# Optimization experiments

Measured on AMD Instinct MI355X. Metric: run time of the kernel, lower is better.

The kernel has to match this reference:

```python
import jax, jax.numpy as jnp
import numpy as np

N_SRC0, N_DST0 = 100000, 20000   # block0: 100k src -> 20k dst
N_DST1 = 4096                    # block1: 20k src -> 4096 dst (seed nodes)


def setup_inputs() -> dict:
    key = jax.random.key(0)
    ks = jax.random.split(key, 8)
    E0, E1 = 640000, 131072
    return {
        "features": jax.random.normal(ks[0], (N_SRC0, 256), jnp.float32),
        "W1": jax.random.normal(ks[1], (256, 256), jnp.float32) * (1.0 / np.sqrt(256)),
        "b1": jnp.zeros((256,), jnp.float32),
        "W2": jax.random.normal(ks[2], (256, 128), jnp.float32) * (1.0 / np.sqrt(256)),
        "b2": jnp.zeros((128,), jnp.float32),
        "src0": jax.random.randint(ks[3], (E0,), 0, N_SRC0, jnp.int32),
        "dst0": jax.random.randint(ks[4], (E0,), 0, N_DST0, jnp.int32),
        "src1": jax.random.randint(ks[5], (E1,), 0, N_DST0, jnp.int32),
        "dst1": jax.random.randint(ks[6], (E1,), 0, N_DST1, jnp.int32),
    }


def _graph_conv(src, dst, n_dst, feat, W, b):
    # DGL GraphConv, norm='both': D_out^{-1/2} gather-sum D_in^{-1/2}, then WX+b.
    n_src = feat.shape[0]
    ones = jnp.ones(src.shape[0], feat.dtype)
    out_deg = jax.ops.segment_sum(ones, src, num_segments=n_src)
    norm_src = jnp.clip(out_deg, 1.0, None) ** -0.5          # [n_src]
    h = feat * norm_src[:, None]
    agg = jax.ops.segment_sum(h[src], dst, num_segments=n_dst)  # sparse SpMM
    in_deg = jax.ops.segment_sum(ones, dst, num_segments=n_dst)
    norm_dst = jnp.clip(in_deg, 1.0, None) ** -0.5           # [n_dst]
    return (agg * norm_dst[:, None]) @ W + b


def reference(features, W1, b1, W2, b2, src0, dst0, src1, dst1):
    x = jax.nn.relu(_graph_conv(src0, dst0, N_DST0, features, W1, b1))
    x = _graph_conv(src1, dst1, N_DST1, x, W2, b2)
    return x
```

## Files before the change

kernel.cpp:

```cpp
#include <hip/hip_runtime.h>
#include <hip/hip_bf16.h>

#define K_DIM 256
#define RSTRIDE 128

typedef short bf16x8 __attribute__((ext_vector_type(8)));
typedef float f32x4 __attribute__((ext_vector_type(4)));

static __device__ __forceinline__ unsigned short f2bf(float x) {
    __hip_bfloat16 b = __float2bfloat16(x);
    return *reinterpret_cast<unsigned short*>(&b);
}
static __device__ __forceinline__ float bflo(unsigned int p) {
    return __uint_as_float(p << 16);
}
static __device__ __forceinline__ float bfhi(unsigned int p) {
    return __uint_as_float(p & 0xffff0000u);
}

__global__ void mega_kernel(
        const int* __restrict__ src0, const int* __restrict__ dst0,
        int* __restrict__ od0, int* __restrict__ cnt0, int* __restrict__ esrc0, int E0,
        const int* __restrict__ src1, const int* __restrict__ dst1,
        int* __restrict__ od1, int* __restrict__ cnt1, int* __restrict__ esrc1, int E1,
        int edgeBlocks,
        const float* __restrict__ feat, unsigned short* __restrict__ h, int total_f,
        int castBlocks,
        const float* __restrict__ W1, uint4* __restrict__ pw1,
        const float* __restrict__ W2, uint4* __restrict__ pw2) {
    const int b = blockIdx.x;
    if (b < edgeBlocks) {
        int i = b * blockDim.x + threadIdx.x;
        if (i < E0) {
            int s = src0[i];
            int d = dst0[i];
            atomicAdd(&od0[s], 1);
            int slot = atomicAdd(&cnt0[d], 1);
            if (slot < RSTRIDE) esrc0[(d << 7) + slot] = s;
        } else if (i < E0 + E1) {
            int e = i - E0;
            int s = src1[e];
            int d = dst1[e];
            atomicAdd(&od1[s], 1);
            int slot = atomicAdd(&cnt1[d], 1);
            if (slot < RSTRIDE) esrc1[(d << 7) + slot] = s;
        }
    } else if (b < edgeBlocks + castBlocks) {
        int idx = ((b - edgeBlocks) * blockDim.x + threadIdx.x) * 8;
        if (idx >= total_f) return;
        const float4 v0 = *reinterpret_cast<const float4*>(feat + idx);
        const float4 v1 = *reinterpret_cast<const float4*>(feat + idx + 4);
        union { ushort4 u4[2]; uint4 u; } o;
        o.u4[0].x = f2bf(v0.x); o.u4[0].y = f2bf(v0.y);
        o.u4[0].z = f2bf(v0.z); o.u4[0].w = f2bf(v0.w);
        o.u4[1].x = f2bf(v1.x); o.u4[1].y = f2bf(v1.y);
        o.u4[1].z = f2bf(v1.z); o.u4[1].w = f2bf(v1.w);
        *reinterpret_cast<uint4*>(h + idx) = o.u;
    } else if (b < edgeBlocks + castBlocks + 32) {
        int idx = (b - edgeBlocks - castBlocks) * blockDim.x + threadIdx.x;
        int lane = idx & 63;
        int kt = (idx >> 6) & 7;
        int nt = idx >> 9;
        int n = nt * 16 + (lane & 15);
        int k = kt * 32 + (lane >> 4) * 8;
        union { unsigned short us[8]; uint4 u; } o;
#pragma unroll
        for (int j = 0; j < 8; ++j) o.us[j] = f2bf(W1[(size_t)(k + j) * 256 + n]);
        pw1[idx] = o.u;
    } else {
        int idx = (b - edgeBlocks - castBlocks - 32) * blockDim.x + threadIdx.x;
        int lane = idx & 63;
        int kt = (idx >> 6) & 7;
        int nt = idx >> 9;
        int n = nt * 16 + (lane & 15);
        int k = kt * 32 + (lane >> 4) * 8;
        union { unsigned short us[8]; uint4 u; } o;
#pragma unroll
        for (int j = 0; j < 8; ++j) o.us[j] = f2bf(W2[(size_t)(k + j) * 128 + n]);
        pw2[idx] = o.u;
    }
}

template <bool NORM>
__global__ __launch_bounds__(256) void gather_bf16_kernel(
        const unsigned short* __restrict__ hfeat, const int* __restrict__ esrc,
        const int* __restrict__ cnt, const int* __restrict__ od,
        unsigned short* __restrict__ aggb, int n_dst) {
    int row = blockIdx.x * (blockDim.x >> 6) + (threadIdx.x >> 6);
    int lane = threadIdx.x & 63;
    if (row >= n_dst) return;
    const int c = cnt[row];
    const int cend = min(c, RSTRIDE);
    const int* __restrict__ ep = esrc + ((size_t)row << 7);
    float a0 = 0.f, a1 = 0.f, a2 = 0.f, a3 = 0.f;
    int i = 0;
    for (; i + 3 < cend; i += 4) {
        int s0 = ep[i];
        int s1 = ep[i + 1];
        int s2 = ep[i + 2];
        int s3 = ep[i + 3];
        float n0 = NORM ? rsqrtf((float)max(od[s0], 1)) : 1.0f;
        float n1 = NORM ? rsqrtf((float)max(od[s1], 1)) : 1.0f;
        float n2 = NORM ? rsqrtf((float)max(od[s2], 1)) : 1.0f;
        float n3 = NORM ? rsqrtf((float)max(od[s3], 1)) : 1.0f;
        const uint2 p0 = *reinterpret_cast<const uint2*>(hfeat + (((size_t)s0) << 8) + lane * 4);
        const uint2 p1 = *reinterpret_cast<const uint2*>(hfeat + (((size_t)s1) << 8) + lane * 4);
        const uint2 p2 = *reinterpret_cast<const uint2*>(hfeat + (((size_t)s2) << 8) + lane * 4);
        const uint2 p3 = *reinterpret_cast<const uint2*>(hfeat + (((size_t)s3) << 8) + lane * 4);
        if (NORM) {
            a0 = fmaf(bflo(p0.x), n0, a0); a1 = fmaf(bfhi(p0.x), n0, a1);
            a2 = fmaf(bflo(p0.y), n0, a2); a3 = fmaf(bfhi(p0.y), n0, a3);
            a0 = fmaf(bflo(p1.x), n1, a0); a1 = fmaf(bfhi(p1.x), n1, a1);
            a2 = fmaf(bflo(p1.y), n1, a2); a3 = fmaf(bfhi(p1.y), n1, a3);
            a0 = fmaf(bflo(p2.x), n2, a0); a1 = fmaf(bfhi(p2.x), n2, a1);
            a2 = fmaf(bflo(p2.y), n2, a2); a3 = fmaf(bfhi(p2.y), n2, a3);
            a0 = fmaf(bflo(p3.x), n3, a0); a1 = fmaf(bfhi(p3.x), n3, a1);
            a2 = fmaf(bflo(p3.y), n3, a2); a3 = fmaf(bfhi(p3.y), n3, a3);
        } else {
            a0 += (bflo(p0.x) + bflo(p1.x)) + (bflo(p2.x) + bflo(p3.x));
            a1 += (bfhi(p0.x) + bfhi(p1.x)) + (bfhi(p2.x) + bfhi(p3.x));
            a2 += (bflo(p0.y) + bflo(p1.y)) + (bflo(p2.y) + bflo(p3.y));
            a3 += (bfhi(p0.y) + bfhi(p1.y)) + (bfhi(p2.y) + bfhi(p3.y));
        }
    }
    for (; i < cend; ++i) {
        int s0 = ep[i];
        float n0 = NORM ? rsqrtf((float)max(od[s0], 1)) : 1.0f;
        const uint2 p0 = *reinterpret_cast<const uint2*>(hfeat + (((size_t)s0) << 8) + lane * 4);
        if (NORM) {
            a0 = fmaf(bflo(p0.x), n0, a0); a1 = fmaf(bfhi(p0.x), n0, a1);
            a2 = fmaf(bflo(p0.y), n0, a2); a3 = fmaf(bfhi(p0.y), n0, a3);
        } else {
            a0 += bflo(p0.x);
            a1 += bfhi(p0.x);
            a2 += bflo(p0.y);
            a3 += bfhi(p0.y);
        }
    }
    float nd = rsqrtf((float)max(c, 1));
    ushort4 o;
    o.x = f2bf(a0 * nd);
    o.y = f2bf(a1 * nd);
    o.z = f2bf(a2 * nd);
    o.w = f2bf(a3 * nd);
    *reinterpret_cast<ushort4*>(aggb + (((size_t)row) << 8) + lane * 4) = o;
}

__global__ __launch_bounds__(256) void gemm0_mfma_kernel(
        const unsigned short* __restrict__ hA, const uint4* __restrict__ pW,
        const float* __restrict__ bias, const int* __restrict__ od1,
        unsigned short* __restrict__ out, int M) {
    const int m0 = blockIdx.x * 16;
    const int w = threadIdx.x >> 6;
    const int lane = threadIdx.x & 63;

    bf16x8 a[8];
    const unsigned short* ap = hA + (size_t)(m0 + (lane & 15)) * K_DIM + (lane >> 4) * 8;
#pragma unroll
    for (int kt = 0; kt < 8; ++kt)
        a[kt] = *reinterpret_cast<const bf16x8*>(ap + kt * 32);

    const int rbase = m0 + (lane >> 4) * 4;
    float nsv[4];
#pragma unroll
    for (int r = 0; r < 4; ++r) nsv[r] = rsqrtf((float)max(od1[rbase + r], 1));

#pragma unroll
    for (int nt = 0; nt < 4; ++nt) {
        const int n0 = w * 64 + nt * 16;
        f32x4 acc = {0.f, 0.f, 0.f, 0.f};
#pragma unroll
        for (int kt = 0; kt < 8; ++kt) {
            bf16x8 b = *reinterpret_cast<const bf16x8*>(&pW[((size_t)(n0 >> 4) * 8 + kt) * 64 + lane]);
            acc = __builtin_amdgcn_mfma_f32_16x16x32_bf16(a[kt], b, acc, 0, 0, 0);
        }
        const int col = n0 + (lane & 15);
        const float bv = bias[col];
#pragma unroll
        for (int r = 0; r < 4; ++r) {
            float v = fmaxf(acc[r] + bv, 0.0f) * nsv[r];
            out[(size_t)(rbase + r) * K_DIM + col] = f2bf(v);
        }
    }
}

__global__ __launch_bounds__(256) void gemm1_mfma_kernel(
        const unsigned short* __restrict__ hA, const uint4* __restrict__ pW,
        const float* __restrict__ bias, float* __restrict__ out, int M) {
    const int m0 = blockIdx.x * 16;
    const int w = threadIdx.x >> 6;
    const int lane = threadIdx.x & 63;

    bf16x8 a[8];
    const unsigned short* ap = hA + (size_t)(m0 + (lane & 15)) * K_DIM + (lane >> 4) * 8;
#pragma unroll
    for (int kt = 0; kt < 8; ++kt)
        a[kt] = *reinterpret_cast<const bf16x8*>(ap + kt * 32);

    const int rbase = m0 + (lane >> 4) * 4;
#pragma unroll
    for (int nt = 0; nt < 2; ++nt) {
        const int n0 = w * 32 + nt * 16;
        f32x4 acc = {0.f, 0.f, 0.f, 0.f};
#pragma unroll
        for (int kt = 0; kt < 8; ++kt) {
            bf16x8 b = *reinterpret_cast<const bf16x8*>(&pW[((size_t)(n0 >> 4) * 8 + kt) * 64 + lane]);
            acc = __builtin_amdgcn_mfma_f32_16x16x32_bf16(a[kt], b, acc, 0, 0, 0);
        }
        const int col = n0 + (lane & 15);
        const float bv = bias[col];
#pragma unroll
        for (int r = 0; r < 4; ++r)
            out[(size_t)(rbase + r) * 128 + col] = acc[r] + bv;
    }
}

__global__ __launch_bounds__(256) void gatherf_kernel(
        const float* __restrict__ feat, const int* __restrict__ esrc,
        const int* __restrict__ cnt, const int* __restrict__ od,
        float* __restrict__ outbuf, int n_dst) {
    int row = blockIdx.x * (blockDim.x >> 6) + (threadIdx.x >> 6);
    int lane = threadIdx.x & 63;
    if (row >= n_dst) return;
    const int c = cnt[row];
    const int cend = min(c, RSTRIDE);
    const int* __restrict__ ep = esrc + ((size_t)row << 7);
    float4 acc = {0.f, 0.f, 0.f, 0.f};
    for (int i = 0; i < cend; ++i) {
        int s0 = ep[i];
        float n0 = rsqrtf((float)max(od[s0], 1));
        const float4 v0 = *reinterpret_cast<const float4*>(feat + (((size_t)s0) << 8) + lane * 4);
        acc.x = fmaf(v0.x, n0, acc.x); acc.y = fmaf(v0.y, n0, acc.y);
        acc.z = fmaf(v0.z, n0, acc.z); acc.w = fmaf(v0.w, n0, acc.w);
    }
    float nd = rsqrtf((float)max(c, 1));
    float4 o = {acc.x * nd, acc.y * nd, acc.z * nd, acc.w * nd};
    *reinterpret_cast<float4*>(outbuf + (((size_t)row) << 8) + lane * 4) = o;
}

__global__ void edges_kernel(const int* __restrict__ src0, const int* __restrict__ dst0,
                             int* __restrict__ od0, int* __restrict__ cnt0,
                             int* __restrict__ esrc0, int E0,
                             const int* __restrict__ src1, const int* __restrict__ dst1,
                             int* __restrict__ od1, int* __restrict__ cnt1,
                             int* __restrict__ esrc1, int E1) {
    int i = blockIdx.x * blockDim.x + threadIdx.x;
    if (i < E0) {
        int s = src0[i];
        int d = dst0[i];
        atomicAdd(&od0[s], 1);
        int slot = atomicAdd(&cnt0[d], 1);
        if (slot < RSTRIDE) esrc0[(d << 7) + slot] = s;
    } else if (i < E0 + E1) {
        int e = i - E0;
        int s = src1[e];
        int d = dst1[e];
        atomicAdd(&od1[s], 1);
        int slot = atomicAdd(&cnt1[d], 1);
        if (slot < RSTRIDE) esrc1[(d << 7) + slot] = s;
    }
}

template <int ROWS, int NCOLS, bool RELU>
__global__ __launch_bounds__(NCOLS) void gemm_kernel(
        const float* __restrict__ A, const float* __restrict__ W,
        const float* __restrict__ bias, float* __restrict__ out, int M) {
    const int row0 = blockIdx.x * ROWS;
    const int c = threadIdx.x;
    const float* __restrict__ Ablk = A + (size_t)row0 * K_DIM;
    const float* __restrict__ Wc = W + c;

    float acc[ROWS];
#pragma unroll
    for (int r = 0; r < ROWS; ++r) acc[r] = 0.0f;

    float w0 = Wc[0];
    float w1 = Wc[NCOLS];
    float w2 = Wc[2 * NCOLS];
    float w3 = Wc[3 * NCOLS];

#pragma unroll 2
    for (int k = 0; k < K_DIM - 4; k += 4) {
        const float* p = Wc + (size_t)(k + 4) * NCOLS;
        float n0 = p[0];
        float n1 = p[NCOLS];
        float n2 = p[2 * NCOLS];
        float n3 = p[3 * NCOLS];
#pragma unroll
        for (int r = 0; r < ROWS; ++r) {
            const float4 a = *reinterpret_cast<const float4*>(Ablk + r * K_DIM + k);
            acc[r] = fmaf(a.x, w0, acc[r]);
            acc[r] = fmaf(a.y, w1, acc[r]);
            acc[r] = fmaf(a.z, w2, acc[r]);
            acc[r] = fmaf(a.w, w3, acc[r]);
        }
        w0 = n0; w1 = n1; w2 = n2; w3 = n3;
    }
    {
        const int k = K_DIM - 4;
#pragma unroll
        for (int r = 0; r < ROWS; ++r) {
            const float4 a = *reinterpret_cast<const float4*>(Ablk + r * K_DIM + k);
            acc[r] = fmaf(a.x, w0, acc[r]);
            acc[r] = fmaf(a.y, w1, acc[r]);
            acc[r] = fmaf(a.z, w2, acc[r]);
            acc[r] = fmaf(a.w, w3, acc[r]);
        }
    }

    const float b = bias[c];
#pragma unroll
    for (int r = 0; r < ROWS; ++r) {
        float v = acc[r] + b;
        if (RELU) v = fmaxf(v, 0.0f);
        out[(size_t)(row0 + r) * NCOLS + c] = v;
    }
}

extern "C" void kernel_launch(void* const* d_in, const int* in_sizes, int n_in,
                              void* d_out, int out_size, void* d_ws, size_t ws_size,
                              hipStream_t stream) {
    const float* features = (const float*)d_in[0];
    const float* W1 = (const float*)d_in[1];
    const float* b1 = (const float*)d_in[2];
    const float* W2 = (const float*)d_in[3];
    const float* b2 = (const float*)d_in[4];
    const int* src0 = (const int*)d_in[5];
    const int* dst0 = (const int*)d_in[6];
    const int* src1 = (const int*)d_in[7];
    const int* dst1 = (const int*)d_in[8];
    const int E0 = in_sizes[5];
    const int E1 = in_sizes[7];
    const int NSRC0 = 100000, NDST0 = 20000, NDST1 = 4096;

    char* ws = (char*)d_ws;
    size_t off = 0;
    auto carve = [&](size_t bytes) -> void* {
        void* p = ws + off;
        off = (off + bytes + 255) & ~(size_t)255;
        return p;
    };
    int* od0  = (int*)carve((size_t)NSRC0 * 4);
    int* od1  = (int*)carve((size_t)NDST0 * 4);
    int* cnt0 = (int*)carve((size_t)NDST0 * 4);
    int* cnt1 = (int*)carve((size_t)NDST1 * 4);
    const size_t zero_span = off;
    uint4* pW1  = (uint4*)carve((size_t)8192 * 16);
    uint4* pW2  = (uint4*)carve((size_t)4096 * 16);
    int* esrc0p = (int*)carve((size_t)NDST0 * RSTRIDE * 4);
    int* esrc1p = (int*)carve((size_t)NDST1 * RSTRIDE * 4);
    unsigned short* aggb = (unsigned short*)carve((size_t)NDST0 * K_DIM * 2);
    const size_t hfeat_bytes = (size_t)NSRC0 * K_DIM * 2;
    const size_t xbufb_bytes = (size_t)NDST0 * K_DIM * 2;
    const size_t agg1b_bytes = (size_t)NDST1 * K_DIM * 2;
    const size_t need_bf16 = off + (hfeat_bytes > xbufb_bytes + agg1b_bytes
                                        ? hfeat_bytes : xbufb_bytes + agg1b_bytes);
    (void)n_in; (void)out_size;

    hipMemsetAsync(ws, 0, zero_span, stream);

    if (ws_size >= need_bf16) {
        unsigned short* hfeat = (unsigned short*)(ws + off);
        unsigned short* xbufb = (unsigned short*)(ws + off);
        unsigned short* agg1b = (unsigned short*)(ws + off + xbufb_bytes);

        const int total_f = NSRC0 * K_DIM;
        const int edgeBlocks = (E0 + E1 + 255) / 256;
        const int castBlocks = (total_f / 8 + 255) / 256;
        mega_kernel<<<edgeBlocks + castBlocks + 48, 256, 0, stream>>>(
            src0, dst0, od0, cnt0, esrc0p, E0,
            src1, dst1, od1, cnt1, esrc1p, E1, edgeBlocks,
            features, hfeat, total_f, castBlocks,
            W1, pW1, W2, pW2);
        gather_bf16_kernel<true><<<(NDST0 + 3) / 4, 256, 0, stream>>>(
            hfeat, esrc0p, cnt0, od0, aggb, NDST0);
        gemm0_mfma_kernel<<<NDST0 / 16, 256, 0, stream>>>(aggb, pW1, b1, od1, xbufb, NDST0);
        gather_bf16_kernel<false><<<(NDST1 + 3) / 4, 256, 0, stream>>>(
            xbufb, esrc1p, cnt1, nullptr, agg1b, NDST1);
        gemm1_mfma_kernel<<<NDST1 / 16, 256, 0, stream>>>(agg1b, pW2, b2,
                                                          (float*)d_out, NDST1);
    } else {
        float* agg0 = (float*)carve((size_t)NDST0 * K_DIM * 4);
        float* xbuf = (float*)carve((size_t)NDST0 * K_DIM * 4);
        float* agg1 = (float*)carve((size_t)NDST1 * K_DIM * 4);
        edges_kernel<<<(E0 + E1 + 255) / 256, 256, 0, stream>>>(
            src0, dst0, od0, cnt0, esrc0p, E0,
            src1, dst1, od1, cnt1, esrc1p, E1);
        gatherf_kernel<<<(NDST0 + 3) / 4, 256, 0, stream>>>(features, esrc0p, cnt0, od0,
                                                            agg0, NDST0);
        gemm_kernel<16, 256, true><<<NDST0 / 16, 256, 0, stream>>>(agg0, W1, b1, xbuf, NDST0);
        gatherf_kernel<<<(NDST1 + 3) / 4, 256, 0, stream>>>(xbuf, esrc1p, cnt1, od1,
                                                            agg1, NDST1);
        gemm_kernel<4, 128, false><<<NDST1 / 4, 128, 0, stream>>>(agg1, W2, b2,
                                                                  (float*)d_out, NDST1);
    }
}
```

Measured before the change: 314.8 us.

## Privatize degree counters and edge lists per XCD with workgroup-scope atomics

```diff
diff --git a/kernel.cpp b/kernel.cpp
--- a/kernel.cpp
+++ b/kernel.cpp
@@ -2,6 +2,8 @@
 #include <hip/hip_bf16.h>
 
 #define K_DIM 256
+#define XCDS 8
+#define PSTRIDE 32
 #define RSTRIDE 128
 
 typedef short bf16x8 __attribute__((ext_vector_type(8)));
@@ -17,33 +19,43 @@
 static __device__ __forceinline__ float bfhi(unsigned int p) {
     return __uint_as_float(p & 0xffff0000u);
 }
+static __device__ __forceinline__ unsigned xcc_id() {
+    unsigned x;
+    asm volatile("s_getreg_b32 %0, hwreg(HW_REG_XCC_ID)" : "=s"(x));
+    return x & 7;
+}
+static __device__ __forceinline__ int l2_atomic_add(int* p) {
+    return __hip_atomic_fetch_add(p, 1, __ATOMIC_RELAXED, __HIP_MEMORY_SCOPE_WORKGROUP);
+}
 
 __global__ void mega_kernel(
         const int* __restrict__ src0, const int* __restrict__ dst0,
-        int* __restrict__ od0, int* __restrict__ cnt0, int* __restrict__ esrc0, int E0,
+        int* __restrict__ od0x, int* __restrict__ cnt0x, int* __restrict__ esrc0, int E0,
         const int* __restrict__ src1, const int* __restrict__ dst1,
-        int* __restrict__ od1, int* __restrict__ cnt1, int* __restrict__ esrc1, int E1,
+        int* __restrict__ od1x, int* __restrict__ cnt1x, int* __restrict__ esrc1, int E1,
         int edgeBlocks,
         const float* __restrict__ feat, unsigned short* __restrict__ h, int total_f,
         int castBlocks,
         const float* __restrict__ W1, uint4* __restrict__ pw1,
         const float* __restrict__ W2, uint4* __restrict__ pw2) {
     const int b = blockIdx.x;
+    const int NSRC0 = 100000, NDST0 = 20000, NDST1 = 4096;
     if (b < edgeBlocks) {
+        const unsigned x = xcc_id();
         int i = b * blockDim.x + threadIdx.x;
         if (i < E0) {
             int s = src0[i];
             int d = dst0[i];
-            atomicAdd(&od0[s], 1);
-            int slot = atomicAdd(&cnt0[d], 1);
-            if (slot < RSTRIDE) esrc0[(d << 7) + slot] = s;
+            l2_atomic_add(&od0x[x * NSRC0 + s]);
+            int slot = l2_atomic_add(&cnt0x[x * NDST0 + d]);
+            if (slot < PSTRIDE) esrc0[(((size_t)(x * NDST0 + d)) << 5) + slot] = s;
         } else if (i < E0 + E1) {
             int e = i - E0;
             int s = src1[e];
             int d = dst1[e];
-            atomicAdd(&od1[s], 1);
-            int slot = atomicAdd(&cnt1[d], 1);
-            if (slot < RSTRIDE) esrc1[(d << 7) + slot] = s;
+            l2_atomic_add(&od1x[x * NDST0 + s]);
+            int slot = l2_atomic_add(&cnt1x[x * NDST1 + d]);
+            if (slot < PSTRIDE) esrc1[(((size_t)(x * NDST1 + d)) << 5) + slot] = s;
         }
     } else if (b < edgeBlocks + castBlocks) {
         int idx = ((b - edgeBlocks) * blockDim.x + threadIdx.x) * 8;
@@ -81,6 +93,23 @@
     }
 }
 
+__global__ void reduce8_kernel(const int* __restrict__ od0x, int* __restrict__ od0s, int n0,
+                               const int* __restrict__ od1x, int* __restrict__ od1s, int n1) {
+    int i = blockIdx.x * blockDim.x + threadIdx.x;
+    if (i < n0) {
+        int s = 0;
+#pragma unroll
+        for (int x = 0; x < XCDS; ++x) s += od0x[x * n0 + i];
+        od0s[i] = s;
+    } else if (i < n0 + n1) {
+        int j = i - n0;
+        int s = 0;
+#pragma unroll
+        for (int x = 0; x < XCDS; ++x) s += od1x[x * n1 + j];
+        od1s[j] = s;
+    }
+}
+
 template <bool NORM>
 __global__ __launch_bounds__(256) void gather_bf16_kernel(
         const unsigned short* __restrict__ hfeat, const int* __restrict__ esrc,
@@ -89,55 +118,59 @@
     int row = blockIdx.x * (blockDim.x >> 6) + (threadIdx.x >> 6);
     int lane = threadIdx.x & 63;
     if (row >= n_dst) return;
-    const int c = cnt[row];
-    const int cend = min(c, RSTRIDE);
-    const int* __restrict__ ep = esrc + ((size_t)row << 7);
     float a0 = 0.f, a1 = 0.f, a2 = 0.f, a3 = 0.f;
-    int i = 0;
-    for (; i + 3 < cend; i += 4) {
-        int s0 = ep[i];
-        int s1 = ep[i + 1];
-        int s2 = ep[i + 2];
-        int s3 = ep[i + 3];
-        float n0 = NORM ? rsqrtf((float)max(od[s0], 1)) : 1.0f;
-        float n1 = NORM ? rsqrtf((float)max(od[s1], 1)) : 1.0f;
-        float n2 = NORM ? rsqrtf((float)max(od[s2], 1)) : 1.0f;
-        float n3 = NORM ? rsqrtf((float)max(od[s3], 1)) : 1.0f;
-        const uint2 p0 = *reinterpret_cast<const uint2*>(hfeat + (((size_t)s0) << 8) + lane * 4);
-        const uint2 p1 = *reinterpret_cast<const uint2*>(hfeat + (((size_t)s1) << 8) + lane * 4);
-        const uint2 p2 = *reinterpret_cast<const uint2*>(hfeat + (((size_t)s2) << 8) + lane * 4);
-        const uint2 p3 = *reinterpret_cast<const uint2*>(hfeat + (((size_t)s3) << 8) + lane * 4);
-        if (NORM) {
-            a0 = fmaf(bflo(p0.x), n0, a0); a1 = fmaf(bfhi(p0.x), n0, a1);
-            a2 = fmaf(bflo(p0.y), n0, a2); a3 = fmaf(bfhi(p0.y), n0, a3);
-            a0 = fmaf(bflo(p1.x), n1, a0); a1 = fmaf(bfhi(p1.x), n1, a1);
-            a2 = fmaf(bflo(p1.y), n1, a2); a3 = fmaf(bfhi(p1.y), n1, a3);
-            a0 = fmaf(bflo(p2.x), n2, a0); a1 = fmaf(bfhi(p2.x), n2, a1);
-            a2 = fmaf(bflo(p2.y), n2, a2); a3 = fmaf(bfhi(p2.y), n2, a3);
-            a0 = fmaf(bflo(p3.x), n3, a0); a1 = fmaf(bfhi(p3.x), n3, a1);
-            a2 = fmaf(bflo(p3.y), n3, a2); a3 = fmaf(bfhi(p3.y), n3, a3);
-        } else {
-            a0 += (bflo(p0.x) + bflo(p1.x)) + (bflo(p2.x) + bflo(p3.x));
-            a1 += (bfhi(p0.x) + bfhi(p1.x)) + (bfhi(p2.x) + bfhi(p3.x));
-            a2 += (bflo(p0.y) + bflo(p1.y)) + (bflo(p2.y) + bflo(p3.y));
-            a3 += (bfhi(p0.y) + bfhi(p1.y)) + (bfhi(p2.y) + bfhi(p3.y));
-        }
-    }
-    for (; i < cend; ++i) {
-        int s0 = ep[i];
-        float n0 = NORM ? rsqrtf((float)max(od[s0], 1)) : 1.0f;
-        const uint2 p0 = *reinterpret_cast<const uint2*>(hfeat + (((size_t)s0) << 8) + lane * 4);
-        if (NORM) {
-            a0 = fmaf(bflo(p0.x), n0, a0); a1 = fmaf(bfhi(p0.x), n0, a1);
-            a2 = fmaf(bflo(p0.y), n0, a2); a3 = fmaf(bfhi(p0.y), n0, a3);
-        } else {
-            a0 += bflo(p0.x);
-            a1 += bfhi(p0.x);
-            a2 += bflo(p0.y);
-            a3 += bfhi(p0.y);
-        }
-    }
-    float nd = rsqrtf((float)max(c, 1));
+    int ctot = 0;
+#pragma unroll
+    for (int x = 0; x < XCDS; ++x) {
+        const int cx = min(cnt[x * n_dst + row], PSTRIDE);
+        ctot += cx;
+        const int* __restrict__ ep = esrc + (((size_t)(x * n_dst + row)) << 5);
+        int i = 0;
+        for (; i + 3 < cx; i += 4) {
+            int s0 = ep[i];
+            int s1 = ep[i + 1];
+            int s2 = ep[i + 2];
+            int s3 = ep[i + 3];
+            float n0 = NORM ? rsqrtf((float)max(od[s0], 1)) : 1.0f;
+            float n1 = NORM ? rsqrtf((float)max(od[s1], 1)) : 1.0f;
+            float n2 = NORM ? rsqrtf((float)max(od[s2], 1)) : 1.0f;
+            float n3 = NORM ? rsqrtf((float)max(od[s3], 1)) : 1.0f;
+            const uint2 p0 = *reinterpret_cast<const uint2*>(hfeat + (((size_t)s0) << 8) + lane * 4);
+            const uint2 p1 = *reinterpret_cast<const uint2*>(hfeat + (((size_t)s1) << 8) + lane * 4);
+            const uint2 p2 = *reinterpret_cast<const uint2*>(hfeat + (((size_t)s2) << 8) + lane * 4);
+            const uint2 p3 = *reinterpret_cast<const uint2*>(hfeat + (((size_t)s3) << 8) + lane * 4);
+            if (NORM) {
+                a0 = fmaf(bflo(p0.x), n0, a0); a1 = fmaf(bfhi(p0.x), n0, a1);
+                a2 = fmaf(bflo(p0.y), n0, a2); a3 = fmaf(bfhi(p0.y), n0, a3);
+                a0 = fmaf(bflo(p1.x), n1, a0); a1 = fmaf(bfhi(p1.x), n1, a1);
+                a2 = fmaf(bflo(p1.y), n1, a2); a3 = fmaf(bfhi(p1.y), n1, a3);
+                a0 = fmaf(bflo(p2.x), n2, a0); a1 = fmaf(bfhi(p2.x), n2, a1);
+                a2 = fmaf(bflo(p2.y), n2, a2); a3 = fmaf(bfhi(p2.y), n2, a3);
+                a0 = fmaf(bflo(p3.x), n3, a0); a1 = fmaf(bfhi(p3.x), n3, a1);
+                a2 = fmaf(bflo(p3.y), n3, a2); a3 = fmaf(bfhi(p3.y), n3, a3);
+            } else {
+                a0 += (bflo(p0.x) + bflo(p1.x)) + (bflo(p2.x) + bflo(p3.x));
+                a1 += (bfhi(p0.x) + bfhi(p1.x)) + (bfhi(p2.x) + bfhi(p3.x));
+                a2 += (bflo(p0.y) + bflo(p1.y)) + (bflo(p2.y) + bflo(p3.y));
+                a3 += (bfhi(p0.y) + bfhi(p1.y)) + (bfhi(p2.y) + bfhi(p3.y));
+            }
+        }
+        for (; i < cx; ++i) {
+            int s0 = ep[i];
+            float n0 = NORM ? rsqrtf((float)max(od[s0], 1)) : 1.0f;
+            const uint2 p0 = *reinterpret_cast<const uint2*>(hfeat + (((size_t)s0) << 8) + lane * 4);
+            if (NORM) {
+                a0 = fmaf(bflo(p0.x), n0, a0); a1 = fmaf(bfhi(p0.x), n0, a1);
+                a2 = fmaf(bflo(p0.y), n0, a2); a3 = fmaf(bfhi(p0.y), n0, a3);
+            } else {
+                a0 += bflo(p0.x);
+                a1 += bfhi(p0.x);
+                a2 += bflo(p0.y);
+                a3 += bfhi(p0.y);
+            }
+        }
+    }
+    float nd = rsqrtf((float)max(ctot, 1));
     ushort4 o;
     o.x = f2bf(a0 * nd);
     o.y = f2bf(a1 * nd);
@@ -213,29 +246,6 @@
         for (int r = 0; r < 4; ++r)
             out[(size_t)(rbase + r) * 128 + col] = acc[r] + bv;
     }
-}
-
-__global__ __launch_bounds__(256) void gatherf_kernel(
-        const float* __restrict__ feat, const int* __restrict__ esrc,
-        const int* __restrict__ cnt, const int* __restrict__ od,
-        float* __restrict__ outbuf, int n_dst) {
-    int row = blockIdx.x * (blockDim.x >> 6) + (threadIdx.x >> 6);
-    int lane = threadIdx.x & 63;
-    if (row >= n_dst) return;
-    const int c = cnt[row];
-    const int cend = min(c, RSTRIDE);
-    const int* __restrict__ ep = esrc + ((size_t)row << 7);
-    float4 acc = {0.f, 0.f, 0.f, 0.f};
-    for (int i = 0; i < cend; ++i) {
-        int s0 = ep[i];
-        float n0 = rsqrtf((float)max(od[s0], 1));
-        const float4 v0 = *reinterpret_cast<const float4*>(feat + (((size_t)s0) << 8) + lane * 4);
-        acc.x = fmaf(v0.x, n0, acc.x); acc.y = fmaf(v0.y, n0, acc.y);
-        acc.z = fmaf(v0.z, n0, acc.z); acc.w = fmaf(v0.w, n0, acc.w);
-    }
-    float nd = rsqrtf((float)max(c, 1));
-    float4 o = {acc.x * nd, acc.y * nd, acc.z * nd, acc.w * nd};
-    *reinterpret_cast<float4*>(outbuf + (((size_t)row) << 8) + lane * 4) = o;
 }
 
 __global__ void edges_kernel(const int* __restrict__ src0, const int* __restrict__ dst0,
@@ -261,6 +271,29 @@
     }
 }
 
+__global__ __launch_bounds__(256) void gatherf_kernel(
+        const float* __restrict__ feat, const int* __restrict__ esrc,
+        const int* __restrict__ cnt, const int* __restrict__ od,
+        float* __restrict__ outbuf, int n_dst) {
+    int row = blockIdx.x * (blockDim.x >> 6) + (threadIdx.x >> 6);
+    int lane = threadIdx.x & 63;
+    if (row >= n_dst) return;
+    const int c = cnt[row];
+    const int cend = min(c, RSTRIDE);
+    const int* __restrict__ ep = esrc + ((size_t)row << 7);
+    float4 acc = {0.f, 0.f, 0.f, 0.f};
+    for (int i = 0; i < cend; ++i) {
+        int s0 = ep[i];
+        float n0 = rsqrtf((float)max(od[s0], 1));
+        const float4 v0 = *reinterpret_cast<const float4*>(feat + (((size_t)s0) << 8) + lane * 4);
+        acc.x = fmaf(v0.x, n0, acc.x); acc.y = fmaf(v0.y, n0, acc.y);
+        acc.z = fmaf(v0.z, n0, acc.z); acc.w = fmaf(v0.w, n0, acc.w);
+    }
+    float nd = rsqrtf((float)max(c, 1));
+    float4 o = {acc.x * nd, acc.y * nd, acc.z * nd, acc.w * nd};
+    *reinterpret_cast<float4*>(outbuf + (((size_t)row) << 8) + lane * 4) = o;
+}
+
 template <int ROWS, int NCOLS, bool RELU>
 __global__ __launch_bounds__(NCOLS) void gemm_kernel(
         const float* __restrict__ A, const float* __restrict__ W,
@@ -340,15 +373,17 @@
         off = (off + bytes + 255) & ~(size_t)255;
         return p;
     };
-    int* od0  = (int*)carve((size_t)NSRC0 * 4);
-    int* od1  = (int*)carve((size_t)NDST0 * 4);
-    int* cnt0 = (int*)carve((size_t)NDST0 * 4);
-    int* cnt1 = (int*)carve((size_t)NDST1 * 4);
+    int* od0x  = (int*)carve((size_t)XCDS * NSRC0 * 4);
+    int* od1x  = (int*)carve((size_t)XCDS * NDST0 * 4);
+    int* cnt0x = (int*)carve((size_t)XCDS * NDST0 * 4);
+    int* cnt1x = (int*)carve((size_t)XCDS * NDST1 * 4);
     const size_t zero_span = off;
+    int* od0s = (int*)carve((size_t)NSRC0 * 4);
+    int* od1s = (int*)carve((size_t)NDST0 * 4);
     uint4* pW1  = (uint4*)carve((size_t)8192 * 16);
     uint4* pW2  = (uint4*)carve((size_t)4096 * 16);
-    int* esrc0p = (int*)carve((size_t)NDST0 * RSTRIDE * 4);
-    int* esrc1p = (int*)carve((size_t)NDST1 * RSTRIDE * 4);
+    int* esrc0p = (int*)carve((size_t)XCDS * NDST0 * PSTRIDE * 4);
+    int* esrc1p = (int*)carve((size_t)XCDS * NDST1 * PSTRIDE * 4);
     unsigned short* aggb = (unsigned short*)carve((size_t)NDST0 * K_DIM * 2);
     const size_t hfeat_bytes = (size_t)NSRC0 * K_DIM * 2;
     const size_t xbufb_bytes = (size_t)NDST0 * K_DIM * 2;
@@ -368,15 +403,17 @@
         const int edgeBlocks = (E0 + E1 + 255) / 256;
         const int castBlocks = (total_f / 8 + 255) / 256;
         mega_kernel<<<edgeBlocks + castBlocks + 48, 256, 0, stream>>>(
-            src0, dst0, od0, cnt0, esrc0p, E0,
-            src1, dst1, od1, cnt1, esrc1p, E1, edgeBlocks,
+            src0, dst0, od0x, cnt0x, esrc0p, E0,
+            src1, dst1, od1x, cnt1x, esrc1p, E1, edgeBlocks,
             features, hfeat, total_f, castBlocks,
             W1, pW1, W2, pW2);
+        reduce8_kernel<<<(NSRC0 + NDST0 + 255) / 256, 256, 0, stream>>>(
+            od0x, od0s, NSRC0, od1x, od1s, NDST0);
         gather_bf16_kernel<true><<<(NDST0 + 3) / 4, 256, 0, stream>>>(
-            hfeat, esrc0p, cnt0, od0, aggb, NDST0);
-        gemm0_mfma_kernel<<<NDST0 / 16, 256, 0, stream>>>(aggb, pW1, b1, od1, xbufb, NDST0);
+            hfeat, esrc0p, cnt0x, od0s, aggb, NDST0);
+        gemm0_mfma_kernel<<<NDST0 / 16, 256, 0, stream>>>(aggb, pW1, b1, od1s, xbufb, NDST0);
         gather_bf16_kernel<false><<<(NDST1 + 3) / 4, 256, 0, stream>>>(
-            xbufb, esrc1p, cnt1, nullptr, agg1b, NDST1);
+            xbufb, esrc1p, cnt1x, nullptr, agg1b, NDST1);
         gemm1_mfma_kernel<<<NDST1 / 16, 256, 0, stream>>>(agg1b, pW2, b2,
                                                           (float*)d_out, NDST1);
     } else {
@@ -384,12 +421,12 @@
         float* xbuf = (float*)carve((size_t)NDST0 * K_DIM * 4);
         float* agg1 = (float*)carve((size_t)NDST1 * K_DIM * 4);
         edges_kernel<<<(E0 + E1 + 255) / 256, 256, 0, stream>>>(
-            src0, dst0, od0, cnt0, esrc0p, E0,
-            src1, dst1, od1, cnt1, esrc1p, E1);
-        gatherf_kernel<<<(NDST0 + 3) / 4, 256, 0, stream>>>(features, esrc0p, cnt0, od0,
+            src0, dst0, od0x, cnt0x, esrc0p, E0,
+            src1, dst1, od1x, cnt1x, esrc1p, E1);
+        gatherf_kernel<<<(NDST0 + 3) / 4, 256, 0, stream>>>(features, esrc0p, cnt0x, od0x,
                                                             agg0, NDST0);
         gemm_kernel<16, 256, true><<<NDST0 / 16, 256, 0, stream>>>(agg0, W1, b1, xbuf, NDST0);
-        gatherf_kernel<<<(NDST1 + 3) / 4, 256, 0, stream>>>(xbuf, esrc1p, cnt1, od1,
+        gatherf_kernel<<<(NDST1 + 3) / 4, 256, 0, stream>>>(xbuf, esrc1p, cnt1x, od1x,
                                                             agg1, NDST1);
         gemm_kernel<4, 128, false><<<NDST1 / 4, 128, 0, stream>>>(agg1, W2, b2,
                                                                   (float*)d_out, NDST1);
```

Result: slower. 358.5 us (+13.9%).
